# Performance work log

Hardware: AMD Instinct MI355X
Metric: run time of the kernel (lower is better)

The kernel has to match this reference:

```python
import jax, jax.numpy as jnp
import numpy as np

N, E, IN_DIM, EDGE_DIM, EMB, H, L = 50000, 800000, 128, 32, 256, 8, 4
C = EMB // H  # per-head channels = 32
NEG_SLOPE = 0.2


def setup_inputs() -> dict:
    key = jax.random.key(0)
    ks = jax.random.split(key, 12)
    s = lambda d: 1.0 / np.sqrt(d)
    return {
        "x": jax.random.normal(ks[0], (N, IN_DIM), jnp.float32),
        "edge_index": jax.random.randint(ks[1], (2, E), 0, N, jnp.int32),
        "edge_attr": jax.random.normal(ks[2], (E, EDGE_DIM), jnp.float32),
        "w_in": jax.random.normal(ks[3], (IN_DIM, EMB), jnp.float32) * s(IN_DIM),
        "b_in": jnp.zeros((EMB,), jnp.float32),
        "W_l": jax.random.normal(ks[4], (L, EMB, EMB), jnp.float32) * s(EMB),
        "We_l": jax.random.normal(ks[5], (L, EDGE_DIM, EMB), jnp.float32) * s(EDGE_DIM),
        "att_src": jax.random.normal(ks[6], (L, H, C), jnp.float32) * s(C),
        "att_dst": jax.random.normal(ks[7], (L, H, C), jnp.float32) * s(C),
        "att_edge": jax.random.normal(ks[8], (L, H, C), jnp.float32) * s(C),
        "bias_l": jnp.zeros((L, EMB), jnp.float32),
        "w_out": jax.random.normal(ks[9], (EMB, 1), jnp.float32) * s(EMB),
        "b_out": jnp.zeros((1,), jnp.float32),
    }


def _gat_forward(x, edge_index, edge_attr, w_in, b_in, W_l, We_l,
                 att_src, att_dst, att_edge, bias_l, w_out, b_out):
    # add self loops (PyG GATConv default, edge_attr fill_value='mean')
    loop = jnp.arange(N, dtype=edge_index.dtype)
    src = jnp.concatenate([edge_index[0], loop])  # [E+N]
    dst = jnp.concatenate([edge_index[1], loop])
    ea = jnp.concatenate([edge_attr,
                          jnp.broadcast_to(edge_attr.mean(0), (N, EDGE_DIM))], 0)

    h = x @ w_in + b_in  # [N, EMB]
    for l in range(L):
        hp = (h @ W_l[l]).reshape(N, H, C)            # [N,H,C]
        ep = (ea @ We_l[l]).reshape(-1, H, C)         # [E+N,H,C]
        a_s = (hp * att_src[l]).sum(-1)               # [N,H]
        a_d = (hp * att_dst[l]).sum(-1)               # [N,H]
        e = a_s[src] + a_d[dst] + (ep * att_edge[l]).sum(-1)  # [E+N,H]
        e = jnp.where(e >= 0, e, NEG_SLOPE * e)
        # segment softmax over incoming edges of each dst node
        m = jax.ops.segment_max(e, dst, num_segments=N)
        e = jnp.exp(e - m[dst])
        denom = jax.ops.segment_sum(e, dst, num_segments=N)
        alpha = e / (denom[dst] + 1e-16)              # [E+N,H]
        msg = hp[src] * alpha[..., None]              # [E+N,H,C]
        h = jax.ops.segment_sum(msg, dst, num_segments=N).reshape(N, EMB) + bias_l[l]
    out = h @ w_out + b_out                           # [N,1]
    return out.squeeze(1)


def reference(x, edge_index, edge_attr, w_in, b_in, W_l, We_l,
              att_src, att_dst, att_edge, bias_l, w_out, b_out):
    return _gat_forward(x, edge_index, edge_attr, w_in, b_in, W_l, We_l,
                        att_src, att_dst, att_edge, bias_l, w_out, b_out)
```

## Files before the change

### kernel.cpp

```cpp
#include <hip/hip_runtime.h>

#define NN 50000
#define MPAD 50048
#define EE 800000
#define ETOT (EE + NN)
#define IN_DIM 128
#define EDGE_DIM 32
#define EMB 256
#define HH 8
#define LL 4
#define NEG_SLOPE 0.2f

typedef __attribute__((ext_vector_type(8))) short bf16x8;
typedef __attribute__((ext_vector_type(4))) float f32x4;

__device__ inline ushort f2bf_rn(float x) {
    union { float f; uint u; } v; v.f = x;
    uint r = v.u + 0x7FFFu + ((v.u >> 16) & 1u);
    return (ushort)(r >> 16);
}
__device__ inline float bf2f(ushort b) {
    union { uint u; float f; } v; v.u = ((uint)b) << 16;
    return v.f;
}

__device__ __forceinline__ void g2l16(const void* g, void* l) {
    __builtin_amdgcn_global_load_lds((const __attribute__((address_space(1))) void*)g,
                                     (__attribute__((address_space(3))) void*)l, 16, 0, 0);
}


__global__ void zero_int_kernel(int* p, int n) {
    int i = blockIdx.x * 256 + threadIdx.x;
    if (i < n) p[i] = 0;
}

__global__ __launch_bounds__(256) void mean_kernel(const float* __restrict__ ea,
                                                   float* __restrict__ accum) {
    __shared__ float part[256];
    int d = threadIdx.x & 31;
    int g = threadIdx.x >> 5;
    float s = 0.f;
    for (int e = blockIdx.x * 8 + g; e < EE; e += gridDim.x * 8)
        s += ea[(size_t)e * 32 + d];
    part[threadIdx.x] = s;
    __syncthreads();
    if (g == 0) {
        float t = part[d];
        for (int k = 1; k < 8; ++k) t += part[k * 32 + d];
        atomicAdd(&accum[d], t);
    }
}

__global__ void precompute_kernel(const float* __restrict__ accum,
                                  const float* __restrict__ We,
                                  const float* __restrict__ att_e,
                                  float* __restrict__ mean_ea,
                                  float* __restrict__ v) {
    int t = threadIdx.x;
    if (t < 32) mean_ea[t] = accum[t] * (1.0f / EE);
    int l = t >> 8, rem = t & 255, d = rem >> 3, hh = rem & 7;
    float s = 0.f;
#pragma unroll
    for (int c = 0; c < 32; ++c)
        s += We[((size_t)(l * 32 + d)) * 256 + hh * 32 + c] * att_e[l * 256 + hh * 32 + c];
    v[t] = s;
}

__global__ void hist_kernel(const int* __restrict__ ei, int* __restrict__ cnt) {
    int i = blockIdx.x * 256 + threadIdx.x;
    if (i >= ETOT) return;
    int dst = (i < EE) ? ei[EE + i] : (i - EE);
    atomicAdd(&cnt[dst], 1);
}

__global__ __launch_bounds__(256) void scan_phase1(const int* __restrict__ cnt,
                                                   int* __restrict__ bsum) {
    int b = blockIdx.x, t = threadIdx.x;
    int i0 = b * 1024 + t * 4;
    int s = 0;
#pragma unroll
    for (int r = 0; r < 4; ++r) s += (i0 + r < NN) ? cnt[i0 + r] : 0;
    for (int off = 1; off < 64; off <<= 1) s += __shfl_xor(s, off);
    __shared__ int wtot[4];
    if ((t & 63) == 0) wtot[t >> 6] = s;
    __syncthreads();
    if (t == 0) bsum[b] = wtot[0] + wtot[1] + wtot[2] + wtot[3];
}

__global__ void scan_phase2(int* __restrict__ bsum, int* __restrict__ row_ptr, int nb) {
    int lane = threadIdx.x;
    int vv = (lane < nb) ? bsum[lane] : 0;
    int incl = vv;
    for (int off = 1; off < 64; off <<= 1) {
        int u = __shfl_up(incl, off);
        if (lane >= off) incl += u;
    }
    if (lane < nb) bsum[lane] = incl - vv;
    if (lane == 0) row_ptr[NN] = ETOT;
}

__global__ __launch_bounds__(256) void scan_phase3(const int* __restrict__ cnt,
                                                   const int* __restrict__ bsum,
                                                   int* __restrict__ row_ptr,
                                                   int* __restrict__ fill) {
    int b = blockIdx.x, t = threadIdx.x;
    int i0 = b * 1024 + t * 4;
    int v[4];
    int s = 0;
#pragma unroll
    for (int r = 0; r < 4; ++r) { v[r] = (i0 + r < NN) ? cnt[i0 + r] : 0; s += v[r]; }
    int lane = t & 63, wv = t >> 6;
    int incl = s;
    for (int off = 1; off < 64; off <<= 1) {
        int u = __shfl_up(incl, off);
        if (lane >= off) incl += u;
    }
    __shared__ int wtot[4];
    if (lane == 63) wtot[wv] = incl;
    __syncthreads();
    int wpref = 0;
    for (int k = 0; k < wv; ++k) wpref += wtot[k];
    int start = bsum[b] + wpref + incl - s;
#pragma unroll
    for (int r = 0; r < 4; ++r) {
        int i = i0 + r;
        if (i < NN) { row_ptr[i] = start; fill[i] = start; }
        start += v[r];
    }
}

__global__ void scatter_kernel(const int* __restrict__ ei, int* __restrict__ fill,
                               int* __restrict__ sorted_src, int* __restrict__ sorted_eid) {
    int i = blockIdx.x * 256 + threadIdx.x;
    if (i >= ETOT) return;
    int dst, src;
    if (i < EE) { src = ei[i]; dst = ei[EE + i]; }
    else        { src = i - EE; dst = i - EE; }
    int pos = atomicAdd(&fill[dst], 1);
    sorted_src[pos] = src;
    sorted_eid[pos] = i;
}

__global__ __launch_bounds__(256) void split_weights(const float* __restrict__ w_in,
                                                     const float* __restrict__ W_l,
                                                     ushort* __restrict__ bh,
                                                     ushort* __restrict__ bl) {
    int t = blockIdx.x * 256 + threadIdx.x;
    if (t >= 32768 + 4 * 65536) return;
    float val;
    size_t dst;
    if (t < 32768) {
        int n = t >> 7, k = t & 127;
        val = w_in[(size_t)k * 256 + n];
        dst = (size_t)n * 128 + k;
    } else {
        int u = t - 32768;
        int l = u >> 16, r = u & 65535;
        int n = r >> 8, k = r & 255;
        val = W_l[(size_t)l * 65536 + (size_t)k * 256 + n];
        dst = 32768 + (size_t)l * 65536 + (size_t)n * 256 + k;
    }
    ushort hi = f2bf_rn(val);
    bh[dst] = hi;
    bl[dst] = f2bf_rn(val - bf2f(hi));
}

__global__ void split_x(const float* __restrict__ x, ushort* __restrict__ xh,
                        ushort* __restrict__ xl) {
    int i = blockIdx.x * 256 + threadIdx.x;
    if (i >= MPAD * 128) return;
    int n = i >> 7;
    float val = (n < NN) ? x[i] : 0.f;
    union { float f; uint u; } uv; uv.f = val;
    ushort hi = (ushort)(uv.u >> 16);
    xh[i] = hi;
    xl[i] = f2bf_rn(val - bf2f(hi));
}

__global__ __launch_bounds__(256) void edge_logits(const float* __restrict__ edge_attr,
                                                   const float* __restrict__ mean_ea,
                                                   const int* __restrict__ sorted_eid,
                                                   const float* __restrict__ v,
                                                   _Float16* __restrict__ e_all) {
    __shared__ float vs[1024];
    for (int t = threadIdx.x; t < 1024; t += 256) vs[t] = v[t];
    __syncthreads();
    int p = blockIdx.x * 256 + threadIdx.x;
    if (p >= ETOT) return;
    int eid = sorted_eid[p];
    const float4* row = (const float4*)((eid < EE) ? (edge_attr + (size_t)eid * 32) : mean_ea);
    float r[32];
#pragma unroll
    for (int q = 0; q < 8; ++q) {
        float4 f = row[q];
        r[q * 4] = f.x; r[q * 4 + 1] = f.y; r[q * 4 + 2] = f.z; r[q * 4 + 3] = f.w;
    }
    float acc[4][8] = {};
#pragma unroll 4
    for (int d = 0; d < 32; ++d) {
        float rv = r[d];
#pragma unroll
        for (int l = 0; l < 4; ++l)
#pragma unroll
            for (int h = 0; h < 8; ++h) acc[l][h] += rv * vs[l * 256 + d * 8 + h];
    }
#pragma unroll
    for (int l = 0; l < 4; ++l) {
        union { uint4 u; _Float16 h[8]; } pk;
#pragma unroll
        for (int h = 0; h < 8; ++h) pk.h[h] = (_Float16)acc[l][h];
        *(uint4*)&e_all[(size_t)l * ETOT * 8 + (size_t)p * 8] = pk.u;
    }
}

template <int MODE>
__global__ __launch_bounds__(256) void gemm_mfma(const ushort* __restrict__ Ah,
                                                 const ushort* __restrict__ Al,
                                                 const ushort* __restrict__ Bh,
                                                 const ushort* __restrict__ Bl,
                                                 const float* __restrict__ bias,
                                                 _Float16* __restrict__ hp_out,
                                                 ushort* __restrict__ hh_out,
                                                 ushort* __restrict__ hl_out,
                                                 int M, int K) {
    __shared__ __align__(16) ushort sAh[8192], sAl[8192], sBh[8192], sBl[8192];
    int tid = threadIdx.x;
    int m0 = blockIdx.x * 128, n0 = blockIdx.y * 128;
    int wid = tid >> 6, lane = tid & 63;
    int wm = wid & 1, wn = wid >> 1;
    int lr = lane & 15, grp = lane >> 4;
    f32x4 acc[4][4];
#pragma unroll
    for (int i = 0; i < 4; ++i)
#pragma unroll
        for (int j = 0; j < 4; ++j) acc[i][j] = (f32x4){0.f, 0.f, 0.f, 0.f};

    for (int k0 = 0; k0 < K; k0 += 64) {
        if (k0) __syncthreads();
#pragma unroll
        for (int i = 0; i < 4; ++i) {
            int ldso = wid * 2048 + i * 512;
            int o = ldso + lane * 8;
            int m = o >> 6;
            int kl = ((((o >> 3) & 7) ^ (m & 7)) << 3) + k0;
            size_t ga = (size_t)(m0 + m) * K + kl;
            size_t gb = (size_t)(n0 + m) * K + kl;
            g2l16(Ah + ga, sAh + ldso);
            g2l16(Al + ga, sAl + ldso);
            g2l16(Bh + gb, sBh + ldso);
            g2l16(Bl + gb, sBl + ldso);
        }
        __syncthreads();
#pragma unroll
        for (int ks = 0; ks < 2; ++ks) {
            bf16x8 vbh[4], vbl[4];
#pragma unroll
            for (int j = 0; j < 4; ++j) {
                int n = wn * 64 + j * 16 + lr;
                int off = n * 64 + ((ks * 32 + grp * 8) ^ ((n & 7) << 3));
                vbh[j] = *(const bf16x8*)&sBh[off];
                vbl[j] = *(const bf16x8*)&sBl[off];
            }
#pragma unroll
            for (int i = 0; i < 4; ++i) {
                int mm = wm * 64 + i * 16 + lr;
                int off = mm * 64 + ((ks * 32 + grp * 8) ^ ((mm & 7) << 3));
                bf16x8 vah = *(const bf16x8*)&sAh[off];
                bf16x8 valo = *(const bf16x8*)&sAl[off];
#pragma unroll
                for (int j = 0; j < 4; ++j) {
                    acc[i][j] = __builtin_amdgcn_mfma_f32_16x16x32_bf16(valo, vbh[j], acc[i][j], 0, 0, 0);
                    acc[i][j] = __builtin_amdgcn_mfma_f32_16x16x32_bf16(vah, vbl[j], acc[i][j], 0, 0, 0);
                    acc[i][j] = __builtin_amdgcn_mfma_f32_16x16x32_bf16(vah, vbh[j], acc[i][j], 0, 0, 0);
                }
            }
        }
    }
#pragma unroll
    for (int j = 0; j < 4; ++j) {
        int c = n0 + wn * 64 + j * 16 + lr;
        float bj = (MODE == 0) ? bias[c] : 0.f;
#pragma unroll
        for (int i = 0; i < 4; ++i) {
            int mb = m0 + wm * 64 + i * 16 + grp * 4;
#pragma unroll
            for (int r = 0; r < 4; ++r) {
                int row = mb + r;
                if (row < M) {
                    float val = acc[i][j][r] + bj;
                    if (MODE == 0) {
                        union { float f; uint u; } uv; uv.f = val;
                        ushort hi = (ushort)(uv.u >> 16);
                        hh_out[(size_t)row * 256 + c] = hi;
                        hl_out[(size_t)row * 256 + c] = f2bf_rn(val - bf2f(hi));
                    } else {
                        hp_out[(size_t)row * 256 + c] = (_Float16)val;
                    }
                }
            }
        }
    }
}


__global__ __launch_bounds__(256) void a_sd_kernel(const _Float16* __restrict__ hp,
                                                   const float* __restrict__ att_s,
                                                   const float* __restrict__ att_d,
                                                   float* __restrict__ a_s,
                                                   float* __restrict__ a_d) {
    int idx = blockIdx.x * 256 + threadIdx.x;
    if (idx >= NN * 8) return;
    int n = idx >> 3, hh = idx & 7;
    const uint4* base = (const uint4*)(hp + (size_t)n * 256 + hh * 32);
    const float4* as4 = (const float4*)(att_s + hh * 32);
    const float4* ad4 = (const float4*)(att_d + hh * 32);
    float ss = 0.f, sd = 0.f;
#pragma unroll
    for (int q = 0; q < 4; ++q) {
        union { uint4 u; _Float16 f[8]; } hv;
        hv.u = base[q];
        float4 s0 = as4[q * 2], s1 = as4[q * 2 + 1];
        float4 d0 = ad4[q * 2], d1 = ad4[q * 2 + 1];
        float f0 = (float)hv.f[0], f1 = (float)hv.f[1], f2 = (float)hv.f[2], f3 = (float)hv.f[3];
        float f4 = (float)hv.f[4], f5 = (float)hv.f[5], f6 = (float)hv.f[6], f7 = (float)hv.f[7];
        ss += f0 * s0.x + f1 * s0.y + f2 * s0.z + f3 * s0.w + f4 * s1.x + f5 * s1.y + f6 * s1.z + f7 * s1.w;
        sd += f0 * d0.x + f1 * d0.y + f2 * d0.z + f3 * d0.w + f4 * d1.x + f5 * d1.y + f6 * d1.z + f7 * d1.w;
    }
    a_s[idx] = ss;
    a_d[idx] = sd;
}

__global__ __launch_bounds__(256) void aggregate_kernel(const _Float16* __restrict__ hp,
                                                        const float* __restrict__ a_s,
                                                        const float* __restrict__ a_d,
                                                        const _Float16* __restrict__ e_l,
                                                        const int* __restrict__ sorted_src,
                                                        const int* __restrict__ row_ptr,
                                                        const float* __restrict__ bias,
                                                        ushort* __restrict__ h_hi,
                                                        ushort* __restrict__ h_lo) {
    int n = (blockIdx.x * 256 + threadIdx.x) >> 6;
    if (n >= NN) return;
    int lane = threadIdx.x & 63;
    int h = lane >> 3;
    int beg = row_ptr[n], end = row_ptr[n + 1];
    float ad = a_d[n * 8 + h];
    float m = -1e30f, s = 0.f;
    float a0 = 0.f, a1 = 0.f, a2 = 0.f, a3 = 0.f;
    int j = beg;
    for (; j + 3 < end; j += 4) {
        int s0 = sorted_src[j], s1 = sorted_src[j + 1];
        int s2 = sorted_src[j + 2], s3 = sorted_src[j + 3];
        float e0 = a_s[s0 * 8 + h] + ad + (float)e_l[(size_t)j * 8 + h];
        float e1 = a_s[s1 * 8 + h] + ad + (float)e_l[(size_t)(j + 1) * 8 + h];
        float e2 = a_s[s2 * 8 + h] + ad + (float)e_l[(size_t)(j + 2) * 8 + h];
        float e3 = a_s[s3 * 8 + h] + ad + (float)e_l[(size_t)(j + 3) * 8 + h];
        union { uint2 u; _Float16 q[4]; } v0, v1, v2, v3;
        v0.u = *(const uint2*)&hp[(size_t)s0 * 256 + lane * 4];
        v1.u = *(const uint2*)&hp[(size_t)s1 * 256 + lane * 4];
        v2.u = *(const uint2*)&hp[(size_t)s2 * 256 + lane * 4];
        v3.u = *(const uint2*)&hp[(size_t)s3 * 256 + lane * 4];
        e0 = (e0 >= 0.f) ? e0 : NEG_SLOPE * e0;
        e1 = (e1 >= 0.f) ? e1 : NEG_SLOPE * e1;
        e2 = (e2 >= 0.f) ? e2 : NEG_SLOPE * e2;
        e3 = (e3 >= 0.f) ? e3 : NEG_SLOPE * e3;
        float nm = fmaxf(m, fmaxf(fmaxf(e0, e1), fmaxf(e2, e3)));
        float sc = __expf(m - nm);
        float w0 = __expf(e0 - nm), w1 = __expf(e1 - nm);
        float w2 = __expf(e2 - nm), w3 = __expf(e3 - nm);
        s = s * sc + ((w0 + w1) + (w2 + w3));
        a0 = a0 * sc + w0 * (float)v0.q[0] + w1 * (float)v1.q[0] + w2 * (float)v2.q[0] + w3 * (float)v3.q[0];
        a1 = a1 * sc + w0 * (float)v0.q[1] + w1 * (float)v1.q[1] + w2 * (float)v2.q[1] + w3 * (float)v3.q[1];
        a2 = a2 * sc + w0 * (float)v0.q[2] + w1 * (float)v1.q[2] + w2 * (float)v2.q[2] + w3 * (float)v3.q[2];
        a3 = a3 * sc + w0 * (float)v0.q[3] + w1 * (float)v1.q[3] + w2 * (float)v2.q[3] + w3 * (float)v3.q[3];
        m = nm;
    }
    for (; j < end; ++j) {
        int src = sorted_src[j];
        float e = a_s[src * 8 + h] + ad + (float)e_l[(size_t)j * 8 + h];
        e = (e >= 0.f) ? e : NEG_SLOPE * e;
        float nm = fmaxf(m, e);
        float sc = __expf(m - nm);
        float w = __expf(e - nm);
        union { uint2 u; _Float16 q[4]; } hv;
        hv.u = *(const uint2*)&hp[(size_t)src * 256 + lane * 4];
        s = s * sc + w;
        a0 = a0 * sc + w * (float)hv.q[0];
        a1 = a1 * sc + w * (float)hv.q[1];
        a2 = a2 * sc + w * (float)hv.q[2];
        a3 = a3 * sc + w * (float)hv.q[3];
        m = nm;
    }
    float inv = 1.0f / (s + 1e-16f);
    float4 b4 = *(const float4*)&bias[lane * 4];
    float o[4] = {a0 * inv + b4.x, a1 * inv + b4.y, a2 * inv + b4.z, a3 * inv + b4.w};
    ushort4 vhi, vlo;
    ushort* ph = (ushort*)&vhi;
    ushort* pl = (ushort*)&vlo;
#pragma unroll
    for (int c = 0; c < 4; ++c) {
        union { float f; uint u; } uv; uv.f = o[c];
        ph[c] = (ushort)(uv.u >> 16);
        pl[c] = f2bf_rn(o[c] - bf2f(ph[c]));
    }
    *(ushort4*)&h_hi[(size_t)n * 256 + lane * 4] = vhi;
    *(ushort4*)&h_lo[(size_t)n * 256 + lane * 4] = vlo;
}

__global__ __launch_bounds__(256) void out_kernel(const ushort* __restrict__ h_hi,
                                                  const ushort* __restrict__ h_lo,
                                                  const float* __restrict__ w_out,
                                                  const float* __restrict__ b_out,
                                                  float* __restrict__ out) {
    int n = (blockIdx.x * 256 + threadIdx.x) >> 6;
    if (n >= NN) return;
    int lane = threadIdx.x & 63;
    union { uint2 u; ushort s[4]; } uh, ul;
    uh.u = *(const uint2*)&h_hi[(size_t)n * 256 + lane * 4];
    ul.u = *(const uint2*)&h_lo[(size_t)n * 256 + lane * 4];
    const float4 wv = *(const float4*)&w_out[lane * 4];
    float s = (bf2f(uh.s[0]) + bf2f(ul.s[0])) * wv.x +
              (bf2f(uh.s[1]) + bf2f(ul.s[1])) * wv.y +
              (bf2f(uh.s[2]) + bf2f(ul.s[2])) * wv.z +
              (bf2f(uh.s[3]) + bf2f(ul.s[3])) * wv.w;
    for (int off = 1; off < 64; off <<= 1) s += __shfl_xor(s, off);
    if (lane == 0) out[n] = s + b_out[0];
}


extern "C" void kernel_launch(void* const* d_in, const int* in_sizes, int n_in,
                              void* d_out, int out_size, void* d_ws, size_t ws_size,
                              hipStream_t stream) {
    const float* x         = (const float*)d_in[0];
    const int*   edge_idx  = (const int*)d_in[1];
    const float* edge_attr = (const float*)d_in[2];
    const float* w_in      = (const float*)d_in[3];
    const float* b_in      = (const float*)d_in[4];
    const float* W_l       = (const float*)d_in[5];
    const float* We_l      = (const float*)d_in[6];
    const float* att_src   = (const float*)d_in[7];
    const float* att_dst   = (const float*)d_in[8];
    const float* att_edge  = (const float*)d_in[9];
    const float* bias_l    = (const float*)d_in[10];
    const float* w_out     = (const float*)d_in[11];
    const float* b_out     = (const float*)d_in[12];
    float* out = (float*)d_out;

    char* ws = (char*)d_ws;
    size_t off = 0;
    auto alloc = [&](size_t bytes) -> void* {
        void* p = ws + off;
        off = (off + bytes + 255) & ~(size_t)255;
        return p;
    };
    ushort*   h_hi       = (ushort*)alloc((size_t)MPAD * 256 * 2);
    ushort*   h_lo       = (ushort*)alloc((size_t)MPAD * 256 * 2);
    _Float16* hp16       = (_Float16*)alloc((size_t)MPAD * 256 * 2);
    float*    a_s        = (float*)alloc((size_t)NN * 8 * 4);
    float*    a_d        = (float*)alloc((size_t)NN * 8 * 4);
    int*      sorted_src = (int*)alloc((size_t)ETOT * 4);
    int*      sorted_eid = (int*)alloc((size_t)ETOT * 4);
    int*      row_ptr    = (int*)alloc((size_t)(NN + 1) * 4);
    int*      fill       = (int*)alloc((size_t)NN * 4);
    int*      cnt        = (int*)alloc((size_t)NN * 4);
    int*      bsum       = (int*)alloc(64 * 4);
    float*    mean_accum = (float*)alloc(32 * 4);
    float*    mean_ea    = (float*)alloc(32 * 4);
    float*    v          = (float*)alloc(1024 * 4);
    ushort*   bsp_hi     = (ushort*)alloc((size_t)294912 * 2);
    ushort*   bsp_lo     = (ushort*)alloc((size_t)294912 * 2);
    char*     uni        = (char*)alloc((size_t)4 * ETOT * 8 * 2);
    ushort*   xh         = (ushort*)uni;
    ushort*   xl         = (ushort*)(uni + (size_t)MPAD * 128 * 2);
    _Float16* e_all      = (_Float16*)uni;

    const int NB = (NN + 1023) / 1024;

    zero_int_kernel<<<(NN + 255) / 256, 256, 0, stream>>>(cnt, NN);
    zero_int_kernel<<<1, 256, 0, stream>>>((int*)mean_accum, 32);
    mean_kernel<<<512, 256, 0, stream>>>(edge_attr, mean_accum);
    precompute_kernel<<<1, 1024, 0, stream>>>(mean_accum, We_l, att_edge, mean_ea, v);
    split_weights<<<(294912 + 255) / 256, 256, 0, stream>>>(w_in, W_l, bsp_hi, bsp_lo);
    split_x<<<(MPAD * 128 + 255) / 256, 256, 0, stream>>>(x, xh, xl);

    dim3 ggrid((NN + 127) / 128, 2);
    gemm_mfma<0><<<ggrid, 256, 0, stream>>>(xh, xl, bsp_hi, bsp_lo, b_in,
                                            nullptr, h_hi, h_lo, NN, IN_DIM);

    hist_kernel<<<(ETOT + 255) / 256, 256, 0, stream>>>(edge_idx, cnt);
    scan_phase1<<<NB, 256, 0, stream>>>(cnt, bsum);
    scan_phase2<<<1, 64, 0, stream>>>(bsum, row_ptr, NB);
    scan_phase3<<<NB, 256, 0, stream>>>(cnt, bsum, row_ptr, fill);
    scatter_kernel<<<(ETOT + 255) / 256, 256, 0, stream>>>(edge_idx, fill, sorted_src, sorted_eid);
    edge_logits<<<(ETOT + 255) / 256, 256, 0, stream>>>(edge_attr, mean_ea, sorted_eid, v, e_all);

    for (int l = 0; l < LL; ++l) {
        const ushort* wh = bsp_hi + 32768 + (size_t)l * 65536;
        const ushort* wl = bsp_lo + 32768 + (size_t)l * 65536;
        gemm_mfma<1><<<ggrid, 256, 0, stream>>>(h_hi, h_lo, wh, wl, nullptr,
                                                hp16, nullptr, nullptr, NN, EMB);
        a_sd_kernel<<<(NN * 8 + 255) / 256, 256, 0, stream>>>(
            hp16, att_src + l * 256, att_dst + l * 256, a_s, a_d);
        aggregate_kernel<<<NN / 4, 256, 0, stream>>>(
            hp16, a_s, a_d, e_all + (size_t)l * ETOT * 8, sorted_src, row_ptr,
            bias_l + l * 256, h_hi, h_lo);
    }

    out_kernel<<<NN / 4, 256, 0, stream>>>(h_hi, h_lo, w_out, b_out, out);
}
```

Baseline: 762.4 us.

## Derive self-loop edge logits from mean of edge logits instead of mean edge_attr

The separate pass that averaged edge_attr is removed. Because the edge logit is linear in edge_attr, each edge_logits block now reduces its per-edge logits and writes a partial sum. A small reduction kernel averages those partials, and a fill kernel writes the self-loop logits at positions recorded during the scatter. This avoids reading edge_attr twice, at the cost of 32 cross-lane shuffle reductions per block, two extra launches, and a slightly different float summation order.

```diff
diff --git a/kernel.cpp b/kernel.cpp
--- a/kernel.cpp
+++ b/kernel.cpp
@@ -35,30 +35,10 @@
     if (i < n) p[i] = 0;
 }
 
-__global__ __launch_bounds__(256) void mean_kernel(const float* __restrict__ ea,
-                                                   float* __restrict__ accum) {
-    __shared__ float part[256];
-    int d = threadIdx.x & 31;
-    int g = threadIdx.x >> 5;
-    float s = 0.f;
-    for (int e = blockIdx.x * 8 + g; e < EE; e += gridDim.x * 8)
-        s += ea[(size_t)e * 32 + d];
-    part[threadIdx.x] = s;
-    __syncthreads();
-    if (g == 0) {
-        float t = part[d];
-        for (int k = 1; k < 8; ++k) t += part[k * 32 + d];
-        atomicAdd(&accum[d], t);
-    }
-}
-
-__global__ void precompute_kernel(const float* __restrict__ accum,
-                                  const float* __restrict__ We,
+__global__ void precompute_kernel(const float* __restrict__ We,
                                   const float* __restrict__ att_e,
-                                  float* __restrict__ mean_ea,
                                   float* __restrict__ v) {
     int t = threadIdx.x;
-    if (t < 32) mean_ea[t] = accum[t] * (1.0f / EE);
     int l = t >> 8, rem = t & 255, d = rem >> 3, hh = rem & 7;
     float s = 0.f;
 #pragma unroll
@@ -131,7 +111,8 @@
 }
 
 __global__ void scatter_kernel(const int* __restrict__ ei, int* __restrict__ fill,
-                               int* __restrict__ sorted_src, int* __restrict__ sorted_eid) {
+                               int* __restrict__ sorted_src, int* __restrict__ sorted_eid,
+                               int* __restrict__ slpos) {
     int i = blockIdx.x * 256 + threadIdx.x;
     if (i >= ETOT) return;
     int dst, src;
@@ -140,6 +121,7 @@
     int pos = atomicAdd(&fill[dst], 1);
     sorted_src[pos] = src;
     sorted_eid[pos] = i;
+    if (i >= EE) slpos[i - EE] = pos;
 }
 
 __global__ __launch_bounds__(256) void split_weights(const float* __restrict__ w_in,
@@ -179,39 +161,95 @@
 }
 
 __global__ __launch_bounds__(256) void edge_logits(const float* __restrict__ edge_attr,
-                                                   const float* __restrict__ mean_ea,
                                                    const int* __restrict__ sorted_eid,
                                                    const float* __restrict__ v,
-                                                   _Float16* __restrict__ e_all) {
+                                                   _Float16* __restrict__ e_all,
+                                                   float* __restrict__ glog_part) {
     __shared__ float vs[1024];
     for (int t = threadIdx.x; t < 1024; t += 256) vs[t] = v[t];
     __syncthreads();
     int p = blockIdx.x * 256 + threadIdx.x;
-    if (p >= ETOT) return;
-    int eid = sorted_eid[p];
-    const float4* row = (const float4*)((eid < EE) ? (edge_attr + (size_t)eid * 32) : mean_ea);
-    float r[32];
-#pragma unroll
-    for (int q = 0; q < 8; ++q) {
-        float4 f = row[q];
-        r[q * 4] = f.x; r[q * 4 + 1] = f.y; r[q * 4 + 2] = f.z; r[q * 4 + 3] = f.w;
-    }
-    float acc[4][8] = {};
+    float acc[4][8];
+#pragma unroll
+    for (int l = 0; l < 4; ++l)
+#pragma unroll
+        for (int h = 0; h < 8; ++h) acc[l][h] = 0.f;
+    if (p < ETOT) {
+        int eid = sorted_eid[p];
+        if (eid < EE) {
+            const float4* row = (const float4*)(edge_attr + (size_t)eid * 32);
+            float r[32];
+#pragma unroll
+            for (int q = 0; q < 8; ++q) {
+                float4 f = row[q];
+                r[q * 4] = f.x; r[q * 4 + 1] = f.y; r[q * 4 + 2] = f.z; r[q * 4 + 3] = f.w;
+            }
 #pragma unroll 4
-    for (int d = 0; d < 32; ++d) {
-        float rv = r[d];
-#pragma unroll
-        for (int l = 0; l < 4; ++l)
-#pragma unroll
-            for (int h = 0; h < 8; ++h) acc[l][h] += rv * vs[l * 256 + d * 8 + h];
-    }
-#pragma unroll
-    for (int l = 0; l < 4; ++l) {
-        union { uint4 u; _Float16 h[8]; } pk;
-#pragma unroll
-        for (int h = 0; h < 8; ++h) pk.h[h] = (_Float16)acc[l][h];
-        *(uint4*)&e_all[(size_t)l * ETOT * 8 + (size_t)p * 8] = pk.u;
-    }
+            for (int d = 0; d < 32; ++d) {
+                float rv = r[d];
+#pragma unroll
+                for (int l = 0; l < 4; ++l)
+#pragma unroll
+                    for (int h = 0; h < 8; ++h) acc[l][h] += rv * vs[l * 256 + d * 8 + h];
+            }
+#pragma unroll
+            for (int l = 0; l < 4; ++l) {
+                union { uint4 u; _Float16 h[8]; } pk;
+#pragma unroll
+                for (int h = 0; h < 8; ++h) pk.h[h] = (_Float16)acc[l][h];
+                *(uint4*)&e_all[(size_t)l * ETOT * 8 + (size_t)p * 8] = pk.u;
+            }
+        }
+    }
+    float* a = &acc[0][0];
+#pragma unroll
+    for (int k = 0; k < 32; ++k)
+        for (int off = 1; off < 64; off <<= 1) a[k] += __shfl_xor(a[k], off);
+    __shared__ float partl[4][32];
+    int lane = threadIdx.x & 63, w = threadIdx.x >> 6;
+    if (lane < 32) partl[w][lane] = a[lane];
+    __syncthreads();
+    if (threadIdx.x < 32)
+        glog_part[(size_t)blockIdx.x * 32 + threadIdx.x] =
+            partl[0][threadIdx.x] + partl[1][threadIdx.x] +
+            partl[2][threadIdx.x] + partl[3][threadIdx.x];
+}
+
+__global__ __launch_bounds__(256) void reduce_glog(const float* __restrict__ part,
+                                                   float* __restrict__ glog, int nblk) {
+    int t = threadIdx.x;
+    int v = t & 31, c = t >> 5;
+    float s = 0.f;
+    for (int b = c; b < nblk; b += 8) s += part[(size_t)b * 32 + v];
+    __shared__ float sm[256];
+    sm[t] = s;
+    __syncthreads();
+    if (c == 0) {
+        float tot = 0.f;
+#pragma unroll
+        for (int k = 0; k < 8; ++k) tot += sm[k * 32 + v];
+        glog[v] = tot * (1.0f / EE);
+    }
+}
+
+__global__ __launch_bounds__(256) void fill_selfloops(const int* __restrict__ slpos,
+                                                      const float* __restrict__ glog,
+                                                      _Float16* __restrict__ e_all) {
+    __shared__ uint4 pk[4];
+    if (threadIdx.x < 4) {
+        int l = threadIdx.x;
+        union { uint4 u; _Float16 h[8]; } q;
+#pragma unroll
+        for (int h = 0; h < 8; ++h) q.h[h] = (_Float16)glog[l * 8 + h];
+        pk[l] = q.u;
+    }
+    __syncthreads();
+    int n = blockIdx.x * 256 + threadIdx.x;
+    if (n >= NN) return;
+    int pos = slpos[n];
+#pragma unroll
+    for (int l = 0; l < 4; ++l)
+        *(uint4*)&e_all[(size_t)l * ETOT * 8 + (size_t)pos * 8] = pk[l];
 }
 
 template <int MODE>
@@ -454,6 +492,8 @@
         off = (off + bytes + 255) & ~(size_t)255;
         return p;
     };
+    const int ELBLK = (ETOT + 255) / 256;
+
     ushort*   h_hi       = (ushort*)alloc((size_t)MPAD * 256 * 2);
     ushort*   h_lo       = (ushort*)alloc((size_t)MPAD * 256 * 2);
     _Float16* hp16       = (_Float16*)alloc((size_t)MPAD * 256 * 2);
@@ -461,13 +501,14 @@
     float*    a_d        = (float*)alloc((size_t)NN * 8 * 4);
     int*      sorted_src = (int*)alloc((size_t)ETOT * 4);
     int*      sorted_eid = (int*)alloc((size_t)ETOT * 4);
+    int*      slpos      = (int*)alloc((size_t)NN * 4);
     int*      row_ptr    = (int*)alloc((size_t)(NN + 1) * 4);
     int*      fill       = (int*)alloc((size_t)NN * 4);
     int*      cnt        = (int*)alloc((size_t)NN * 4);
     int*      bsum       = (int*)alloc(64 * 4);
-    float*    mean_accum = (float*)alloc(32 * 4);
-    float*    mean_ea    = (float*)alloc(32 * 4);
     float*    v          = (float*)alloc(1024 * 4);
+    float*    glog_part  = (float*)alloc((size_t)ELBLK * 32 * 4);
+    float*    glog       = (float*)alloc(32 * 4);
     ushort*   bsp_hi     = (ushort*)alloc((size_t)294912 * 2);
     ushort*   bsp_lo     = (ushort*)alloc((size_t)294912 * 2);
     char*     uni        = (char*)alloc((size_t)4 * ETOT * 8 * 2);
@@ -478,9 +519,7 @@
     const int NB = (NN + 1023) / 1024;
 
     zero_int_kernel<<<(NN + 255) / 256, 256, 0, stream>>>(cnt, NN);
-    zero_int_kernel<<<1, 256, 0, stream>>>((int*)mean_accum, 32);
-    mean_kernel<<<512, 256, 0, stream>>>(edge_attr, mean_accum);
-    precompute_kernel<<<1, 1024, 0, stream>>>(mean_accum, We_l, att_edge, mean_ea, v);
+    precompute_kernel<<<1, 1024, 0, stream>>>(We_l, att_edge, v);
     split_weights<<<(294912 + 255) / 256, 256, 0, stream>>>(w_in, W_l, bsp_hi, bsp_lo);
     split_x<<<(MPAD * 128 + 255) / 256, 256, 0, stream>>>(x, xh, xl);
 
@@ -492,8 +531,11 @@
     scan_phase1<<<NB, 256, 0, stream>>>(cnt, bsum);
     scan_phase2<<<1, 64, 0, stream>>>(bsum, row_ptr, NB);
     scan_phase3<<<NB, 256, 0, stream>>>(cnt, bsum, row_ptr, fill);
-    scatter_kernel<<<(ETOT + 255) / 256, 256, 0, stream>>>(edge_idx, fill, sorted_src, sorted_eid);
-    edge_logits<<<(ETOT + 255) / 256, 256, 0, stream>>>(edge_attr, mean_ea, sorted_eid, v, e_all);
+    scatter_kernel<<<(ETOT + 255) / 256, 256, 0, stream>>>(edge_idx, fill, sorted_src,
+                                                           sorted_eid, slpos);
+    edge_logits<<<ELBLK, 256, 0, stream>>>(edge_attr, sorted_eid, v, e_all, glog_part);
+    reduce_glog<<<1, 256, 0, stream>>>(glog_part, glog, ELBLK);
+    fill_selfloops<<<(NN + 255) / 256, 256, 0, stream>>>(slpos, glog, e_all);
 
     for (int l = 0; l < LL; ++l) {
         const ushort* wh = bsp_hi + 32768 + (size_t)l * 65536;
```

After: 825.4 us. 8.3% more time.
